# Performance work log

Measured on AMD Instinct MI355X. Metric: run time of the kernel, lower is better.

The kernel has to match this reference:

```python
import jax, jax.numpy as jnp
import numpy as np

D_MODEL = 256; N_HEADS = 8; N_LEVELS = 4; N_POINTS = 4; D_FFN = 1024
SHAPES = [(128, 128), (64, 64), (32, 32), (16, 16)]  # (H, W) per level, strides 8/16/32/64 of 1024x1024 input
B = 8; LQ = 1024
S_TOT = sum(h * w for h, w in SHAPES)


def setup_inputs() -> dict:
    key = jax.random.key(0)
    ks = iter(jax.random.split(key, 48))
    d = D_MODEL

    def f(shape, s=0.02):
        return jax.random.normal(next(ks), shape, dtype=jnp.float32) * s

    return {
        'tgt': f((B, LQ, d), 1.0),
        'query_pos': f((B, LQ, d), 1.0),
        'reference_points': jax.random.uniform(next(ks), (B, LQ, N_LEVELS, 2), dtype=jnp.float32),
        'src': f((B, S_TOT, d), 1.0),
        'w_in': f((3 * d, d)), 'b_in': jnp.zeros((3 * d,), jnp.float32),
        'w_out': f((d, d)), 'b_out': jnp.zeros((d,), jnp.float32),
        'ln1_g': jnp.ones((d,), jnp.float32), 'ln1_b': jnp.zeros((d,), jnp.float32),
        'ln2_g': jnp.ones((d,), jnp.float32), 'ln2_b': jnp.zeros((d,), jnp.float32),
        'ln3_g': jnp.ones((d,), jnp.float32), 'ln3_b': jnp.zeros((d,), jnp.float32),
        'w_val': f((d, d)), 'b_val': jnp.zeros((d,), jnp.float32),
        'w_off': f((N_HEADS * N_LEVELS * N_POINTS * 2, d), 0.002),
        'b_off': f((N_HEADS * N_LEVELS * N_POINTS * 2,), 0.5),
        'w_attw': f((N_HEADS * N_LEVELS * N_POINTS, d)),
        'b_attw': jnp.zeros((N_HEADS * N_LEVELS * N_POINTS,), jnp.float32),
        'w_oc': f((d, d)), 'b_oc': jnp.zeros((d,), jnp.float32),
        'w1': f((D_FFN, d)), 'b1': jnp.zeros((D_FFN,), jnp.float32),
        'w2': f((d, D_FFN)), 'b2': jnp.zeros((d,), jnp.float32),
        'spatial_shapes': jnp.array(SHAPES, dtype=jnp.int32),
    }


def layer_norm(x, g, b):
    mu = x.mean(-1, keepdims=True)
    var = ((x - mu) ** 2).mean(-1, keepdims=True)
    return (x - mu) * jax.lax.rsqrt(var + 1e-5) * g + b


def mha(tgt, query_pos, w_in, b_in, w_out, b_out):
    d = D_MODEL; Dh = d // N_HEADS
    Bs, Lq, _ = tgt.shape
    qk = tgt + query_pos
    q = (qk @ w_in[:d].T + b_in[:d]).reshape(Bs, Lq, N_HEADS, Dh)
    k = (qk @ w_in[d:2 * d].T + b_in[d:2 * d]).reshape(Bs, Lq, N_HEADS, Dh)
    v = (tgt @ w_in[2 * d:].T + b_in[2 * d:]).reshape(Bs, Lq, N_HEADS, Dh)
    attn = jax.nn.softmax(jnp.einsum('bqhd,bkhd->bhqk', q, k) / np.sqrt(Dh).astype(np.float32), axis=-1)
    o = jnp.einsum('bhqk,bkhd->bqhd', attn, v).reshape(Bs, Lq, d)
    return o @ w_out.T + b_out


def ms_deform_attn(value, loc, attw):
    # value [B,S,H,Dh]; loc [B,Lq,H,L,P,2] in [0,1]; attw [B,Lq,H,L,P]
    Bs, _, Hh, Dh = value.shape
    Lq = loc.shape[1]

    def to_hfirst(x):  # [B,Lq,Hh,P] -> [B,Hh,Lq*P,1]
        return jnp.transpose(x, (0, 2, 1, 3)).reshape(Bs, Hh, Lq * N_POINTS, 1)

    acc = jnp.zeros((Bs, Hh, Lq * N_POINTS, Dh), value.dtype)
    start = 0
    for l, (H_, W_) in enumerate(SHAPES):
        v = jnp.transpose(value[:, start:start + H_ * W_], (0, 2, 1, 3))  # [B,Hh,HW,Dh]
        start += H_ * W_
        ll = loc[:, :, :, l]  # [B,Lq,Hh,P,2]
        x = ll[..., 0] * W_ - 0.5
        y = ll[..., 1] * H_ - 0.5
        x0 = jnp.floor(x); y0 = jnp.floor(y)
        tx = x - x0; ty = y - y0

        def gather(xi, yi):
            valid = ((xi >= 0) & (xi < W_) & (yi >= 0) & (yi < H_)).astype(value.dtype)
            fi = (jnp.clip(yi, 0, H_ - 1) * W_ + jnp.clip(xi, 0, W_ - 1)).astype(jnp.int32)
            g = jnp.take_along_axis(v, to_hfirst(fi.astype(jnp.float32)).astype(jnp.int32), axis=2)
            return g * to_hfirst(valid)

        samp = (gather(x0, y0) * to_hfirst((1 - tx) * (1 - ty))
                + gather(x0 + 1, y0) * to_hfirst(tx * (1 - ty))
                + gather(x0, y0 + 1) * to_hfirst((1 - tx) * ty)
                + gather(x0 + 1, y0 + 1) * to_hfirst(tx * ty))
        acc = acc + samp * to_hfirst(attw[:, :, :, l])
    out = acc.reshape(Bs, Hh, Lq, N_POINTS, Dh).sum(3)  # [B,Hh,Lq,Dh]
    return jnp.transpose(out, (0, 2, 1, 3)).reshape(Bs, Lq, Hh * Dh)


def reference(tgt, query_pos, reference_points, src, w_in, b_in, w_out, b_out,
              ln1_g, ln1_b, ln2_g, ln2_b, ln3_g, ln3_b,
              w_val, b_val, w_off, b_off, w_attw, b_attw, w_oc, b_oc,
              w1, b1, w2, b2, spatial_shapes):
    Bs, Lq, d = tgt.shape
    Dh = d // N_HEADS
    # --- self attention (q=k=tgt+pos, v=tgt), residual + norm2 ---
    t2 = mha(tgt, query_pos, w_in, b_in, w_out, b_out)
    tgt = layer_norm(tgt + t2, ln2_g, ln2_b)
    # --- MSDeformAttn cross attention, residual + norm1 ---
    query = tgt + query_pos
    value = (src @ w_val.T + b_val).reshape(Bs, -1, N_HEADS, Dh)
    off = (query @ w_off.T + b_off).reshape(Bs, Lq, N_HEADS, N_LEVELS, N_POINTS, 2)
    aw = jax.nn.softmax((query @ w_attw.T + b_attw).reshape(Bs, Lq, N_HEADS, N_LEVELS * N_POINTS), axis=-1)
    aw = aw.reshape(Bs, Lq, N_HEADS, N_LEVELS, N_POINTS)
    normalizer = jnp.array([[w, h] for h, w in SHAPES], dtype=tgt.dtype)  # (W,H) per level
    loc = reference_points[:, :, None, :, None, :] + off / normalizer[None, None, None, :, None, :]
    ca = ms_deform_attn(value, loc, aw) @ w_oc.T + b_oc
    tgt = layer_norm(tgt + ca, ln1_g, ln1_b)
    # --- FFN, residual + norm3 ---
    t2 = jax.nn.relu(tgt @ w1.T + b1) @ w2.T + b2
    tgt = layer_norm(tgt + t2, ln3_g, ln3_b)
    return tgt
```

## Files before the change

### kernel.cpp

```cpp
#include <hip/hip_runtime.h>

typedef unsigned short ushort_t;
typedef unsigned int uint_t;
typedef __attribute__((ext_vector_type(8))) short short8;
typedef __attribute__((ext_vector_type(4))) float floatx4;
typedef __attribute__((ext_vector_type(4))) unsigned short ushortx4;

__device__ __forceinline__ ushort_t f2bf(float f){
  uint_t u = __builtin_bit_cast(uint_t, f);
  u += 0x7FFFu + ((u >> 16) & 1u);
  return (ushort_t)(u >> 16);
}
__device__ __forceinline__ float bf2f(ushort_t u){
  uint_t x = ((uint_t)u) << 16;
  return __builtin_bit_cast(float, x);
}
__device__ __forceinline__ uint_t packbf2(float a, float b){
  return (uint_t)f2bf(a) | ((uint_t)f2bf(b) << 16);
}

__device__ __forceinline__ void gload16(const void* g, void* l){
  __builtin_amdgcn_global_load_lds(
      (const __attribute__((address_space(1))) void*)g,
      (__attribute__((address_space(3))) void*)l, 16, 0, 0);
}

#define FENCED_BARRIER() asm volatile("s_barrier" ::: "memory")

__global__ __launch_bounds__(256) void convert_w_kernel(const float* __restrict__ w_in_v,
    const float* __restrict__ w_val, const float* __restrict__ w_out,
    const float* __restrict__ w_oc, const float* __restrict__ w1,
    const float* __restrict__ w2, ushort_t* __restrict__ dst){
  int j = (blockIdx.x*256 + threadIdx.x) * 4;
  if (j >= 786432) return;
  const float* src; int off;
  if      (j <  65536){ src = w_in_v; off = 0;      }
  else if (j < 131072){ src = w_val;  off = 65536;  }
  else if (j < 196608){ src = w_out;  off = 131072; }
  else if (j < 262144){ src = w_oc;   off = 196608; }
  else if (j < 524288){ src = w1;     off = 262144; }
  else                { src = w2;     off = 524288; }
  float4 v = *(const float4*)(src + (j - off));
  uint2 u; u.x = packbf2(v.x, v.y); u.y = packbf2(v.z, v.w);
  *(uint2*)(dst + j) = u;
}

__global__ __launch_bounds__(256) void pack_offattw_kernel(const float* __restrict__ w_off,
    const float* __restrict__ w_attw, const float* __restrict__ b_off,
    const float* __restrict__ b_attw, float* __restrict__ dst){
  int j = (blockIdx.x*256 + threadIdx.x) * 4;
  if (j >= 98688) return;
  const float* src; int off;
  if      (j < 65536){ src = w_off;  off = 0;     }
  else if (j < 98304){ src = w_attw; off = 65536; }
  else if (j < 98560){ src = b_off;  off = 98304; }
  else               { src = b_attw; off = 98560; }
  *(float4*)(dst + j) = *(const float4*)(src + (j - off));
}

__global__ __launch_bounds__(256) void addln_kernel(const float* __restrict__ X,
    const float* __restrict__ Y, const float* __restrict__ gw,
    const float* __restrict__ bw, float* __restrict__ Out){
  int wave = threadIdx.x >> 6, lane = threadIdx.x & 63;
  long row = (long)blockIdx.x * 4 + wave;
  long base = row * 256 + lane * 4;
  float4 x = *(const float4*)(X + base);
  float4 y = *(const float4*)(Y + base);
  float v0=x.x+y.x, v1=x.y+y.y, v2=x.z+y.z, v3=x.w+y.w;
  float s  = v0+v1+v2+v3;
  float sq = v0*v0+v1*v1+v2*v2+v3*v3;
  #pragma unroll
  for (int off=32; off>0; off>>=1){
    s  += __shfl_xor(s, off);
    sq += __shfl_xor(sq, off);
  }
  float mu  = s * (1.f/256.f);
  float var = sq * (1.f/256.f) - mu*mu;
  float rs  = rsqrtf(var + 1e-5f);
  float4 g4 = *(const float4*)(gw + lane*4);
  float4 b4 = *(const float4*)(bw + lane*4);
  float4 o;
  o.x = (v0-mu)*rs*g4.x + b4.x;
  o.y = (v1-mu)*rs*g4.y + b4.y;
  o.z = (v2-mu)*rs*g4.z + b4.z;
  o.w = (v3-mu)*rs*g4.w + b4.w;
  *(float4*)(Out + base) = o;
}

__device__ __forceinline__ void stage_store(ushort_t* ls, int r, int c4, float4 v){
  int byte = r*64 + ((((c4>>1) ^ ((r>>1)&3)) << 4) | ((c4&1) << 3));
  uint2 u; u.x = packbf2(v.x, v.y); u.y = packbf2(v.z, v.w);
  *(uint2*)((char*)ls + byte) = u;
}
__device__ __forceinline__ void stage_copy16(ushort_t* ls, int r, int s, short8 v){
  int byte = r*64 + ((s ^ ((r>>1)&3)) << 4);
  *(short8*)((char*)ls + byte) = v;
}
__device__ __forceinline__ short8 frag_load(const ushort_t* ls, int r, int g){
  int byte = r*64 + ((g ^ ((r>>1)&3)) << 4);
  return *(const short8*)((const char*)ls + byte);
}

__device__ __forceinline__ short8 frag_load_f32(const float* ls, int r, int g){
  const char* base = (const char*)ls + r*128;
  int x = r & 7;
  float4 f0 = *(const float4*)(base + ((((2*g)  ^ x)) << 4));
  float4 f1 = *(const float4*)(base + ((((2*g+1)^ x)) << 4));
  uint4 u;
  u.x = packbf2(f0.x, f0.y); u.y = packbf2(f0.z, f0.w);
  u.z = packbf2(f1.x, f1.y); u.w = packbf2(f1.z, f1.w);
  return __builtin_bit_cast(short8, u);
}

template<bool RELU, bool OUT_BF16>
__global__ __launch_bounds__(256) void gemm_dma3_kernel(const float* __restrict__ A,
    const ushort_t* __restrict__ Wbf, const float* __restrict__ bias,
    void* __restrict__ Cout, int M, int N, int K){
  __shared__ float    ldsA[2][2048];
  __shared__ ushort_t ldsB[2][4096];
  const int t = threadIdx.x;
  const int lane = t & 63, wave = t >> 6;
  const int wm = wave >> 1, wn = wave & 1;
  const long rowA0 = (long)blockIdx.x * 64;
  const long rowB0 = (long)blockIdx.y * 128;
  const int rr = lane & 15, g = lane >> 4;
  const int arow_in = lane >> 3;
  const int aslot   = (lane & 7) ^ (arow_in & 7);
  const int brow_in = lane >> 2;
  const int bslot   = lane & 3;
  floatx4 acc[2][4] = {};
  const int nsteps = K >> 5;

  #define ISSUE3(kk, buf) do { \
    _Pragma("unroll") \
    for (int c=0;c<2;++c){ \
      int ar_ = wave*16 + c*8 + arow_in; \
      gload16(A + (rowA0 + ar_)*(long)K + (kk) + aslot*4, \
              &ldsA[buf][(wave*16 + c*8)*32]); \
    } \
    _Pragma("unroll") \
    for (int c=0;c<2;++c){ \
      int br_ = wave*32 + c*16 + brow_in; \
      const ushort_t* bs_ = Wbf + (rowB0 + br_)*(long)K + (kk) + (bslot ^ ((br_>>1)&3))*8; \
      gload16(bs_, (char*)ldsB[buf] + (wave*32 + c*16)*64); \
    } \
  } while(0)

  ISSUE3(0, 0);
  if (nsteps > 1) ISSUE3(32, 1);

  for (int k = 0; k < nsteps; ++k){
    if (k < nsteps-1) asm volatile("s_waitcnt vmcnt(4)" ::: "memory");
    else              asm volatile("s_waitcnt vmcnt(0)" ::: "memory");
    FENCED_BARRIER();
    const float*    lA = ldsA[k & 1];
    const ushort_t* lB = ldsB[k & 1];
    short8 af[2], bfr[4];
    #pragma unroll
    for (int mi=0;mi<2;++mi) af[mi]  = frag_load_f32(lA, wm*32 + mi*16 + rr, g);
    #pragma unroll
    for (int ni=0;ni<4;++ni) bfr[ni] = frag_load(lB, wn*64 + ni*16 + rr, g);
    #pragma unroll
    for (int mi=0;mi<2;++mi)
      #pragma unroll
      for (int ni=0;ni<4;++ni)
        acc[mi][ni] = __builtin_amdgcn_mfma_f32_16x16x32_bf16(af[mi], bfr[ni], acc[mi][ni], 0, 0, 0);
    FENCED_BARRIER();
    if (k + 2 < nsteps) ISSUE3((k+2)*32, k & 1);
  }
  #undef ISSUE3

  const int cg = lane >> 4;
  #pragma unroll
  for (int ni=0;ni<4;++ni){
    long n = rowB0 + wn*64 + ni*16 + (lane & 15);
    float bv = bias[n];
    #pragma unroll
    for (int mi=0;mi<2;++mi){
      long m = rowA0 + wm*32 + mi*16 + cg*4;
      #pragma unroll
      for (int r2=0;r2<4;++r2){
        float v = acc[mi][ni][r2] + bv;
        if (RELU) v = fmaxf(v, 0.f);
        if (OUT_BF16) ((ushort_t*)Cout)[(m+r2)*N + n] = f2bf(v);
        else          ((float*)Cout)[(m+r2)*N + n] = v;
      }
    }
  }
}

template<bool RELU, bool OUT_BF16>
__global__ __launch_bounds__(512, 4) void gemm_dma2_kernel(const float* __restrict__ A,
    const ushort_t* __restrict__ Wbf, const float* __restrict__ bias,
    void* __restrict__ Cout, int M, int N, int K){
  __shared__ float    ldsA[2][4096];
  __shared__ ushort_t ldsB[2][8192];
  const int t = threadIdx.x;
  const int lane = t & 63, wave = t >> 6;
  const int wm = wave >> 2, wn = wave & 3;
  const long rowA0 = (long)blockIdx.x * 128;
  const long n0 = (long)blockIdx.y * 256;
  const int rr = lane & 15, g = lane >> 4;
  const int arow_in = lane >> 3;
  const int aslot   = (lane & 7) ^ (arow_in & 7);
  const int brow_in = lane >> 2;
  const int bslot   = lane & 3;
  floatx4 acc[4][4] = {};
  const int nsteps = K >> 5;

  #define ISSUE2(kk, buf) do { \
    _Pragma("unroll") \
    for (int c=0;c<2;++c){ \
      int ar_ = (wave*2 + c)*8 + arow_in; \
      gload16(A + (rowA0 + ar_)*(long)K + (kk) + aslot*4, \
              &ldsA[buf][(wave*2 + c)*8*32]); \
    } \
    _Pragma("unroll") \
    for (int c=0;c<2;++c){ \
      int br_ = (wave*2 + c)*16 + brow_in; \
      const ushort_t* bs_ = Wbf + (n0 + br_)*(long)K + (kk) + (bslot ^ ((br_>>1)&3))*8; \
      gload16(bs_, (char*)ldsB[buf] + (wave*2 + c)*16*64); \
    } \
  } while(0)

  ISSUE2(0, 0);
  if (nsteps > 1) ISSUE2(32, 1);

  for (int k = 0; k < nsteps; ++k){
    if (k < nsteps-1) asm volatile("s_waitcnt vmcnt(4)" ::: "memory");
    else              asm volatile("s_waitcnt vmcnt(0)" ::: "memory");
    FENCED_BARRIER();
    const float*    lA = ldsA[k & 1];
    const ushort_t* lB = ldsB[k & 1];
    short8 af[4], bfr[4];
    #pragma unroll
    for (int mi=0;mi<4;++mi) af[mi]  = frag_load_f32(lA, wm*64 + mi*16 + rr, g);
    #pragma unroll
    for (int ni=0;ni<4;++ni) bfr[ni] = frag_load(lB, wn*64 + ni*16 + rr, g);
    #pragma unroll
    for (int mi=0;mi<4;++mi)
      #pragma unroll
      for (int ni=0;ni<4;++ni)
        acc[mi][ni] = __builtin_amdgcn_mfma_f32_16x16x32_bf16(af[mi], bfr[ni], acc[mi][ni], 0, 0, 0);
    FENCED_BARRIER();
    if (k + 2 < nsteps) ISSUE2((k+2)*32, k & 1);
  }
  #undef ISSUE2

  const int cg = lane >> 4;
  #pragma unroll
  for (int ni=0;ni<4;++ni){
    long n = n0 + wn*64 + ni*16 + (lane & 15);
    float bv = bias[n];
    #pragma unroll
    for (int mi=0;mi<4;++mi){
      long m = rowA0 + wm*64 + mi*16 + cg*4;
      #pragma unroll
      for (int r2=0;r2<4;++r2){
        float v = acc[mi][ni][r2] + bv;
        if (RELU) v = fmaxf(v, 0.f);
        if (OUT_BF16) ((ushort_t*)Cout)[(m+r2)*N + n] = f2bf(v);
        else          ((float*)Cout)[(m+r2)*N + n] = v;
      }
    }
  }
}

template<bool RELU, bool OUT_BF16>
__global__ __launch_bounds__(256) void gemm_add2_kernel(const float* __restrict__ A,
    const float* __restrict__ A2, const float* __restrict__ W,
    const float* __restrict__ bias, void* __restrict__ Cout,
    int M, int N, int K){
  __shared__ ushort_t lsA[4096], lsB[4096];
  const int t = threadIdx.x;
  const int lane = t & 63, wave = t >> 6;
  const int wm = wave >> 1, wn = wave & 1;
  const long rowA0 = (long)blockIdx.x * 128;
  const long rowB0 = (long)blockIdx.y * 128;
  floatx4 acc[4][4] = {};
  const int rr = lane & 15, g = lane >> 4;
  const int rA = t >> 3, c4 = t & 7;
  const float* Ap = A + (rowA0 + rA)*(long)K + c4*4;
  const float* A2p = A2 + (rowA0 + rA)*(long)K + c4*4;
  const float* Wp = W + (rowB0 + rA)*(long)K + c4*4;

  for (int k0 = 0; k0 < K; k0 += 32){
    __syncthreads();
    #pragma unroll
    for (int j=0;j<4;++j){
      float4 v = *(const float4*)(Ap + k0 + (long)(32*j)*K);
      float4 y = *(const float4*)(A2p + k0 + (long)(32*j)*K);
      v.x+=y.x; v.y+=y.y; v.z+=y.z; v.w+=y.w;
      stage_store(lsA, rA + 32*j, c4, v);
      stage_store(lsB, rA + 32*j, c4, *(const float4*)(Wp + k0 + (long)(32*j)*K));
    }
    __syncthreads();
    short8 af[4], bfr[4];
    #pragma unroll
    for (int mi=0;mi<4;++mi) af[mi]  = frag_load(lsA, wm*64 + mi*16 + rr, g);
    #pragma unroll
    for (int ni=0;ni<4;++ni) bfr[ni] = frag_load(lsB, wn*64 + ni*16 + rr, g);
    #pragma unroll
    for (int mi=0;mi<4;++mi)
      #pragma unroll
      for (int ni=0;ni<4;++ni)
        acc[mi][ni] = __builtin_amdgcn_mfma_f32_16x16x32_bf16(af[mi], bfr[ni], acc[mi][ni], 0, 0, 0);
  }
  const int cg = lane >> 4;
  #pragma unroll
  for (int ni=0;ni<4;++ni){
    long n = rowB0 + wn*64 + ni*16 + (lane & 15);
    float bv = bias[n];
    #pragma unroll
    for (int mi=0;mi<4;++mi){
      long m = rowA0 + wm*64 + mi*16 + cg*4;
      #pragma unroll
      for (int r2=0;r2<4;++r2){
        float v = acc[mi][ni][r2] + bv;
        if (RELU) v = fmaxf(v, 0.f);
        if (OUT_BF16) ((ushort_t*)Cout)[(m+r2)*N + n] = f2bf(v);
        else          ((float*)Cout)[(m+r2)*N + n] = v;
      }
    }
  }
}

__global__ __launch_bounds__(256) void attn_mfma_kernel(const ushort_t* __restrict__ QK,
    const ushort_t* __restrict__ V, float* __restrict__ O){
  __shared__ ushort_t lsQ[4096];
  __shared__ ushort_t lsK[1024];
  __shared__ ushort_t lsVT[1024];
  __shared__ ushort_t lsP[4096];
  const int bh = blockIdx.y, b = bh >> 3, h = bh & 7;
  const int qt0 = blockIdx.x * 128;
  const int t = threadIdx.x, lane = t & 63, w = t >> 6;
  const int rr = lane & 15, g = lane >> 4;
  const float csc = 0.25506332f;

  const ushort_t* qbase = QK + ((long)b*1024 + qt0)*512 + h*32;
  #pragma unroll
  for (int j=0;j<2;++j){
    int i = t + j*256; int r = i>>2, s = i&3;
    short8 v = *(const short8*)(qbase + (long)r*512 + s*8);
    stage_copy16(lsQ, r, s, v);
  }
  __syncthreads();
  short8 bq[2];
  bq[0] = frag_load(lsQ, w*32 + rr, g);
  bq[1] = frag_load(lsQ, w*32 + 16 + rr, g);

  floatx4 accO[2][2] = {};
  float rsum[2] = {0.f, 0.f};
  const ushort_t* kbase = QK + (long)b*1024*512 + 256 + h*32;
  const ushort_t* vbase = V  + (long)b*1024*256 + h*32;

  for (int kt = 0; kt < 1024; kt += 32){
    __syncthreads();
    if (t < 128){
      int r = t >> 2, s = t & 3;
      short8 v = *(const short8*)(kbase + (long)(kt + r)*512 + s*8);
      stage_copy16(lsK, r, s, v);
    }
    {
      int kk = t >> 3, d4 = t & 7;
      ushortx4 vv = *(const ushortx4*)(vbase + (long)(kt + kk)*256 + d4*4);
      #pragma unroll
      for (int j=0;j<4;++j){
        int d = d4*4 + j;
        int cb = kk*2;
        int byte = d*64 + ((((cb>>4) ^ ((d>>1)&3)) << 4) | (cb & 15));
        *(ushort_t*)((char*)lsVT + byte) = vv[j];
      }
    }
    __syncthreads();
    floatx4 accS[2][2] = {};
    short8 ak0 = frag_load(lsK, rr, g);
    short8 ak1 = frag_load(lsK, 16 + rr, g);
    accS[0][0] = __builtin_amdgcn_mfma_f32_16x16x32_bf16(ak0, bq[0], accS[0][0], 0,0,0);
    accS[0][1] = __builtin_amdgcn_mfma_f32_16x16x32_bf16(ak0, bq[1], accS[0][1], 0,0,0);
    accS[1][0] = __builtin_amdgcn_mfma_f32_16x16x32_bf16(ak1, bq[0], accS[1][0], 0,0,0);
    accS[1][1] = __builtin_amdgcn_mfma_f32_16x16x32_bf16(ak1, bq[1], accS[1][1], 0,0,0);
    #pragma unroll
    for (int mi=0;mi<2;++mi){
      #pragma unroll
      for (int ni=0;ni<2;++ni){
        float p0 = exp2f(accS[mi][ni][0]*csc);
        float p1 = exp2f(accS[mi][ni][1]*csc);
        float p2 = exp2f(accS[mi][ni][2]*csc);
        float p3 = exp2f(accS[mi][ni][3]*csc);
        rsum[ni] += (p0+p1)+(p2+p3);
        int q   = w*32 + ni*16 + rr;
        int k0b = (mi*16 + g*4)*2;
        int byte = q*64 + ((((k0b>>4) ^ ((q>>1)&3)) << 4) | (k0b & 15));
        uint2 u; u.x = packbf2(p0,p1); u.y = packbf2(p2,p3);
        *(uint2*)((char*)lsP + byte) = u;
      }
    }
    short8 av0 = frag_load(lsVT, rr, g);
    short8 av1 = frag_load(lsVT, 16 + rr, g);
    short8 bp0 = frag_load(lsP, w*32 + rr, g);
    short8 bp1 = frag_load(lsP, w*32 + 16 + rr, g);
    accO[0][0] = __builtin_amdgcn_mfma_f32_16x16x32_bf16(av0, bp0, accO[0][0], 0,0,0);
    accO[0][1] = __builtin_amdgcn_mfma_f32_16x16x32_bf16(av0, bp1, accO[0][1], 0,0,0);
    accO[1][0] = __builtin_amdgcn_mfma_f32_16x16x32_bf16(av1, bp0, accO[1][0], 0,0,0);
    accO[1][1] = __builtin_amdgcn_mfma_f32_16x16x32_bf16(av1, bp1, accO[1][1], 0,0,0);
  }
  #pragma unroll
  for (int ni=0;ni<2;++ni){
    rsum[ni] += __shfl_xor(rsum[ni], 16);
    rsum[ni] += __shfl_xor(rsum[ni], 32);
    float inv = 1.f / rsum[ni];
    int q = qt0 + w*32 + ni*16 + rr;
    float* op = O + ((long)b*1024 + q)*256 + h*32;
    #pragma unroll
    for (int mi=0;mi<2;++mi){
      #pragma unroll
      for (int r2=0;r2<4;++r2){
        int d = mi*16 + g*4 + r2;
        op[d] = accO[mi][ni][r2] * inv;
      }
    }
  }
}

__global__ __launch_bounds__(256) void deform_kernel(const ushort_t* __restrict__ val,
    const float* __restrict__ offaw, const float* __restrict__ refp,
    float* __restrict__ Out){
  __shared__ float s_cat[1536], s_ref[32];
  const int t = threadIdx.x;
  const long q0 = (long)blockIdx.x * 4;
  const float* srcOA = offaw + q0*384;
  *(float4*)(s_cat + t*4) = *(const float4*)(srcOA + t*4);
  if (t < 128) *(float4*)(s_cat + 1024 + t*4) = *(const float4*)(srcOA + 1024 + t*4);
  if (t < 32)  s_ref[t] = refp[q0*8 + t];
  __syncthreads();
  const int qi = t >> 6, tl = t & 63;
  const int h = tl >> 3, dq = (tl & 7) << 2;
  const int bq = (int)q0 + qi;
  const int b = bq >> 10;
  const float* offp = s_cat + qi*384 + h*32;
  const float* awp  = s_cat + qi*384 + 256 + h*16;
  const float* refq = s_ref + qi*8;
  float mx = -1e30f;
  #pragma unroll
  for (int i=0;i<16;++i) mx = fmaxf(mx, awp[i]);
  float p[16], sum = 0.f;
  #pragma unroll
  for (int i=0;i<16;++i){ p[i] = expf(awp[i]-mx); sum += p[i]; }
  float inv = 1.f/sum;
  const long vb = (long)b*21760*256 + h*32 + dq;
  const int Dim[4] = {128,64,32,16};
  const int St[4]  = {0,16384,20480,21504};
  float a0=0.f, a1=0.f, a2=0.f, a3=0.f;
  #pragma unroll
  for (int l=0;l<4;++l){
    const int Wl = Dim[l], Hl = Dim[l], st = St[l];
    float rx = refq[2*l], ry = refq[2*l+1];
    #pragma unroll
    for (int pp=0;pp<4;++pp){
      float x = rx*(float)Wl + offp[l*8+pp*2]   - 0.5f;
      float y = ry*(float)Hl + offp[l*8+pp*2+1] - 0.5f;
      float xf = floorf(x), yf = floorf(y);
      int x0 = (int)xf, y0 = (int)yf;
      float tx = x - xf, ty = y - yf;
      float s0=0.f,s1=0.f,s2=0.f,s3=0.f;
      #define CORNER(XI, YI, WGT) { \
        int xi_ = (XI), yi_ = (YI); \
        bool valid_ = (xi_ >= 0) & (xi_ < Wl) & (yi_ >= 0) & (yi_ < Hl); \
        int xc_ = min(max(xi_, 0), Wl-1), yc_ = min(max(yi_, 0), Hl-1); \
        ushortx4 u = *(const ushortx4*)(val + vb + (long)(st + yc_*Wl + xc_)*256); \
        float wq = valid_ ? (WGT) : 0.f; \
        s0 += wq*bf2f(u[0]); s1 += wq*bf2f(u[1]); \
        s2 += wq*bf2f(u[2]); s3 += wq*bf2f(u[3]); \
      }
      CORNER(x0,   y0,   (1.f-tx)*(1.f-ty));
      CORNER(x0+1, y0,   tx*(1.f-ty));
      CORNER(x0,   y0+1, (1.f-tx)*ty);
      CORNER(x0+1, y0+1, tx*ty);
      #undef CORNER
      float pw = p[l*4+pp];
      a0 += pw*s0; a1 += pw*s1; a2 += pw*s2; a3 += pw*s3;
    }
  }
  float4 o; o.x=a0*inv; o.y=a1*inv; o.z=a2*inv; o.w=a3*inv;
  *(float4*)(Out + (long)bq*256 + h*32 + dq) = o;
}

extern "C" void kernel_launch(void* const* d_in, const int* in_sizes, int n_in,
                              void* d_out, int out_size, void* d_ws, size_t ws_size,
                              hipStream_t stream){
  (void)in_sizes; (void)n_in; (void)out_size; (void)ws_size;
  const float* tgt   = (const float*)d_in[0];
  const float* qpos  = (const float*)d_in[1];
  const float* refp  = (const float*)d_in[2];
  const float* src   = (const float*)d_in[3];
  const float* w_in  = (const float*)d_in[4];
  const float* b_in  = (const float*)d_in[5];
  const float* w_out = (const float*)d_in[6];
  const float* b_out = (const float*)d_in[7];
  const float* ln1g  = (const float*)d_in[8];
  const float* ln1b  = (const float*)d_in[9];
  const float* ln2g  = (const float*)d_in[10];
  const float* ln2b  = (const float*)d_in[11];
  const float* ln3g  = (const float*)d_in[12];
  const float* ln3b  = (const float*)d_in[13];
  const float* w_val = (const float*)d_in[14];
  const float* b_val = (const float*)d_in[15];
  const float* w_off = (const float*)d_in[16];
  const float* b_off = (const float*)d_in[17];
  const float* w_attw= (const float*)d_in[18];
  const float* b_attw= (const float*)d_in[19];
  const float* w_oc  = (const float*)d_in[20];
  const float* b_oc  = (const float*)d_in[21];
  const float* w1    = (const float*)d_in[22];
  const float* b1    = (const float*)d_in[23];
  const float* w2    = (const float*)d_in[24];
  const float* b2    = (const float*)d_in[25];

  float* ws = (float*)d_ws;
  ushort_t* bufQK = (ushort_t*)(ws + 2097152);
  float* bufOA  = ws + 2097152;
  ushort_t* bufV = (ushort_t*)(ws + 6291456);
  float* bufO   = ws + 8388608;
  float* bufT2  = ws + 10485760;
  float* bufTg1 = ws + 12582912;
  float* bufTg2 = ws + 14680064;
  ushort_t* bufVal = (ushort_t*)(ws + 16777216);
  float* bufH   = ws + 16777216;
  ushort_t* bufWbf = (ushort_t*)(ws + 39059456);
  float* bufWOA = ws + 39452672;
  float* outF   = (float*)d_out;

  const ushort_t* winvbf = bufWbf;
  const ushort_t* wvalbf = bufWbf + 65536;
  const ushort_t* woutbf = bufWbf + 131072;
  const ushort_t* wocbf  = bufWbf + 196608;
  const ushort_t* w1bf   = bufWbf + 262144;
  const ushort_t* w2bf   = bufWbf + 524288;

  dim3 B256(256), B512(512);
  convert_w_kernel<<<dim3(768), B256, 0, stream>>>(w_in + 512*256, w_val, w_out, w_oc, w1, w2, bufWbf);
  pack_offattw_kernel<<<dim3(97), B256, 0, stream>>>(w_off, w_attw, b_off, b_attw, bufWOA);
  gemm_add2_kernel<false,true><<<dim3(64,4), B256, 0, stream>>>(tgt, qpos, w_in, b_in, bufQK, 8192, 512, 256);
  gemm_dma3_kernel<false,true><<<dim3(128,2), B256, 0, stream>>>(tgt, winvbf, b_in + 512, bufV, 8192, 256, 256);
  attn_mfma_kernel<<<dim3(8,64), B256, 0, stream>>>(bufQK, bufV, bufO);
  gemm_dma3_kernel<false,false><<<dim3(128,2), B256, 0, stream>>>(bufO, woutbf, b_out, bufT2, 8192, 256, 256);
  addln_kernel<<<dim3(2048), B256, 0, stream>>>(tgt, bufT2, ln2g, ln2b, bufTg1);
  gemm_dma2_kernel<false,true><<<dim3(1360,1), B512, 0, stream>>>(src, wvalbf, b_val, bufVal, 174080, 256, 256);
  gemm_add2_kernel<false,false><<<dim3(64,3), B256, 0, stream>>>(bufTg1, qpos, bufWOA, bufWOA + 98304, bufOA, 8192, 384, 256);
  deform_kernel<<<dim3(2048), B256, 0, stream>>>(bufVal, bufOA, refp, bufO);
  gemm_dma3_kernel<false,false><<<dim3(128,2), B256, 0, stream>>>(bufO, wocbf, b_oc, bufT2, 8192, 256, 256);
  addln_kernel<<<dim3(2048), B256, 0, stream>>>(bufTg1, bufT2, ln1g, ln1b, bufTg2);
  gemm_dma2_kernel<true,false><<<dim3(64,4), B512, 0, stream>>>(bufTg2, w1bf, b1, bufH, 8192, 1024, 256);
  gemm_dma3_kernel<false,false><<<dim3(128,2), B256, 0, stream>>>(bufH, w2bf, b2, bufT2, 8192, 256, 1024);
  addln_kernel<<<dim3(2048), B256, 0, stream>>>(bufTg2, bufT2, ln3g, ln3b, outF);
}
```

Baseline: 290.9 us.

## Replace GEMM kernels with triple-buffered 64-row DMA GEMM and bf16 pre-converted weights

Replaces the 512-thread double-buffered GEMM with a 256-thread, 64-row-tile, triple-buffered variant for the value projection and FFN1. It also drops the register-staged gemm_add2 path: tgt+pos sums now go through a separate elementwise add kernel, and all weights (including in-proj and offset/attention-weight projections) are pre-converted to bf16 so the DMA GEMM can be used everywhere. The goal is deeper load pipelining and more blocks for latency hiding. The cost is extra add-kernel launches and extra global traffic for the materialised sums.

```diff
diff --git a/kernel.cpp b/kernel.cpp
--- a/kernel.cpp
+++ b/kernel.cpp
@@ -27,35 +27,43 @@
 
 #define FENCED_BARRIER() asm volatile("s_barrier" ::: "memory")
 
-__global__ __launch_bounds__(256) void convert_w_kernel(const float* __restrict__ w_in_v,
+__global__ __launch_bounds__(256) void convert_w_kernel(const float* __restrict__ w_in,
     const float* __restrict__ w_val, const float* __restrict__ w_out,
     const float* __restrict__ w_oc, const float* __restrict__ w1,
-    const float* __restrict__ w2, ushort_t* __restrict__ dst){
+    const float* __restrict__ w2, const float* __restrict__ w_off,
+    const float* __restrict__ w_attw, ushort_t* __restrict__ dst){
   int j = (blockIdx.x*256 + threadIdx.x) * 4;
-  if (j >= 786432) return;
+  if (j >= 1015808) return;
   const float* src; int off;
-  if      (j <  65536){ src = w_in_v; off = 0;      }
-  else if (j < 131072){ src = w_val;  off = 65536;  }
-  else if (j < 196608){ src = w_out;  off = 131072; }
-  else if (j < 262144){ src = w_oc;   off = 196608; }
-  else if (j < 524288){ src = w1;     off = 262144; }
-  else                { src = w2;     off = 524288; }
+  if      (j < 196608){ src = w_in;   off = 0;      }
+  else if (j < 262144){ src = w_val;  off = 196608; }
+  else if (j < 327680){ src = w_out;  off = 262144; }
+  else if (j < 393216){ src = w_oc;   off = 327680; }
+  else if (j < 655360){ src = w1;     off = 393216; }
+  else if (j < 917504){ src = w2;     off = 655360; }
+  else if (j < 983040){ src = w_off;  off = 917504; }
+  else                { src = w_attw; off = 983040; }
   float4 v = *(const float4*)(src + (j - off));
   uint2 u; u.x = packbf2(v.x, v.y); u.y = packbf2(v.z, v.w);
   *(uint2*)(dst + j) = u;
 }
 
-__global__ __launch_bounds__(256) void pack_offattw_kernel(const float* __restrict__ w_off,
-    const float* __restrict__ w_attw, const float* __restrict__ b_off,
+__global__ __launch_bounds__(256) void pack_bias_kernel(const float* __restrict__ b_off,
     const float* __restrict__ b_attw, float* __restrict__ dst){
-  int j = (blockIdx.x*256 + threadIdx.x) * 4;
-  if (j >= 98688) return;
-  const float* src; int off;
-  if      (j < 65536){ src = w_off;  off = 0;     }
-  else if (j < 98304){ src = w_attw; off = 65536; }
-  else if (j < 98560){ src = b_off;  off = 98304; }
-  else               { src = b_attw; off = 98560; }
-  *(float4*)(dst + j) = *(const float4*)(src + (j - off));
+  int t = threadIdx.x;
+  dst[t] = b_off[t];
+  if (t < 128) dst[256 + t] = b_attw[t];
+}
+
+__global__ __launch_bounds__(256) void add_kernel(const float* __restrict__ a,
+    const float* __restrict__ b, float* __restrict__ c, int n4){
+  int i = blockIdx.x * 256 + threadIdx.x;
+  if (i < n4){
+    float4 x = ((const float4*)a)[i];
+    float4 y = ((const float4*)b)[i];
+    float4 z; z.x=x.x+y.x; z.y=x.y+y.y; z.z=x.z+y.z; z.w=x.w+y.w;
+    ((float4*)c)[i] = z;
+  }
 }
 
 __global__ __launch_bounds__(256) void addln_kernel(const float* __restrict__ X,
@@ -87,11 +95,6 @@
   *(float4*)(Out + base) = o;
 }
 
-__device__ __forceinline__ void stage_store(ushort_t* ls, int r, int c4, float4 v){
-  int byte = r*64 + ((((c4>>1) ^ ((r>>1)&3)) << 4) | ((c4&1) << 3));
-  uint2 u; u.x = packbf2(v.x, v.y); u.y = packbf2(v.z, v.w);
-  *(uint2*)((char*)ls + byte) = u;
-}
 __device__ __forceinline__ void stage_copy16(ushort_t* ls, int r, int s, short8 v){
   int byte = r*64 + ((s ^ ((r>>1)&3)) << 4);
   *(short8*)((char*)ls + byte) = v;
@@ -190,16 +193,15 @@
 }
 
 template<bool RELU, bool OUT_BF16>
-__global__ __launch_bounds__(512, 4) void gemm_dma2_kernel(const float* __restrict__ A,
+__global__ __launch_bounds__(256) void gemm_dma4_kernel(const float* __restrict__ A,
     const ushort_t* __restrict__ Wbf, const float* __restrict__ bias,
     void* __restrict__ Cout, int M, int N, int K){
-  __shared__ float    ldsA[2][4096];
-  __shared__ ushort_t ldsB[2][8192];
+  __shared__ float    ldsA[3][2048];
+  __shared__ ushort_t ldsB[3][8192];
   const int t = threadIdx.x;
   const int lane = t & 63, wave = t >> 6;
-  const int wm = wave >> 2, wn = wave & 3;
-  const long rowA0 = (long)blockIdx.x * 128;
-  const long n0 = (long)blockIdx.y * 256;
+  const long rowA0 = (long)blockIdx.x * 64;
+  const long rowB0 = (long)blockIdx.y * 256;
   const int rr = lane & 15, g = lane >> 4;
   const int arow_in = lane >> 3;
   const int aslot   = (lane & 7) ^ (arow_in & 7);
@@ -208,112 +210,57 @@
   floatx4 acc[4][4] = {};
   const int nsteps = K >> 5;
 
-  #define ISSUE2(kk, buf) do { \
+  #define ISSUE4(kk, buf) do { \
     _Pragma("unroll") \
     for (int c=0;c<2;++c){ \
-      int ar_ = (wave*2 + c)*8 + arow_in; \
+      int ar_ = wave*16 + c*8 + arow_in; \
       gload16(A + (rowA0 + ar_)*(long)K + (kk) + aslot*4, \
-              &ldsA[buf][(wave*2 + c)*8*32]); \
+              &ldsA[buf][(wave*16 + c*8)*32]); \
     } \
     _Pragma("unroll") \
-    for (int c=0;c<2;++c){ \
-      int br_ = (wave*2 + c)*16 + brow_in; \
-      const ushort_t* bs_ = Wbf + (n0 + br_)*(long)K + (kk) + (bslot ^ ((br_>>1)&3))*8; \
-      gload16(bs_, (char*)ldsB[buf] + (wave*2 + c)*16*64); \
+    for (int c=0;c<4;++c){ \
+      int br_ = wave*64 + c*16 + brow_in; \
+      const ushort_t* bs_ = Wbf + (rowB0 + br_)*(long)K + (kk) + (bslot ^ ((br_>>1)&3))*8; \
+      gload16(bs_, (char*)ldsB[buf] + (wave*64 + c*16)*64); \
     } \
   } while(0)
 
-  ISSUE2(0, 0);
-  if (nsteps > 1) ISSUE2(32, 1);
+  ISSUE4(0, 0);
+  if (nsteps > 1) ISSUE4(32, 1);
+  if (nsteps > 2) ISSUE4(64, 2);
 
   for (int k = 0; k < nsteps; ++k){
-    if (k < nsteps-1) asm volatile("s_waitcnt vmcnt(4)" ::: "memory");
-    else              asm volatile("s_waitcnt vmcnt(0)" ::: "memory");
+    int ahead = nsteps - 1 - k; if (ahead > 2) ahead = 2;
+    if (ahead == 2)      asm volatile("s_waitcnt vmcnt(12)" ::: "memory");
+    else if (ahead == 1) asm volatile("s_waitcnt vmcnt(6)"  ::: "memory");
+    else                 asm volatile("s_waitcnt vmcnt(0)"  ::: "memory");
     FENCED_BARRIER();
-    const float*    lA = ldsA[k & 1];
-    const ushort_t* lB = ldsB[k & 1];
+    int bsel = k % 3;
+    const float*    lA = ldsA[bsel];
+    const ushort_t* lB = ldsB[bsel];
     short8 af[4], bfr[4];
     #pragma unroll
-    for (int mi=0;mi<4;++mi) af[mi]  = frag_load_f32(lA, wm*64 + mi*16 + rr, g);
-    #pragma unroll
-    for (int ni=0;ni<4;++ni) bfr[ni] = frag_load(lB, wn*64 + ni*16 + rr, g);
+    for (int mi=0;mi<4;++mi) af[mi]  = frag_load_f32(lA, mi*16 + rr, g);
+    #pragma unroll
+    for (int ni=0;ni<4;++ni) bfr[ni] = frag_load(lB, wave*64 + ni*16 + rr, g);
     #pragma unroll
     for (int mi=0;mi<4;++mi)
       #pragma unroll
       for (int ni=0;ni<4;++ni)
         acc[mi][ni] = __builtin_amdgcn_mfma_f32_16x16x32_bf16(af[mi], bfr[ni], acc[mi][ni], 0, 0, 0);
     FENCED_BARRIER();
-    if (k + 2 < nsteps) ISSUE2((k+2)*32, k & 1);
-  }
-  #undef ISSUE2
+    if (k + 3 < nsteps) ISSUE4((k+3)*32, bsel);
+  }
+  #undef ISSUE4
 
   const int cg = lane >> 4;
   #pragma unroll
   for (int ni=0;ni<4;++ni){
-    long n = n0 + wn*64 + ni*16 + (lane & 15);
+    long n = rowB0 + wave*64 + ni*16 + (lane & 15);
     float bv = bias[n];
     #pragma unroll
     for (int mi=0;mi<4;++mi){
-      long m = rowA0 + wm*64 + mi*16 + cg*4;
-      #pragma unroll
-      for (int r2=0;r2<4;++r2){
-        float v = acc[mi][ni][r2] + bv;
-        if (RELU) v = fmaxf(v, 0.f);
-        if (OUT_BF16) ((ushort_t*)Cout)[(m+r2)*N + n] = f2bf(v);
-        else          ((float*)Cout)[(m+r2)*N + n] = v;
-      }
-    }
-  }
-}
-
-template<bool RELU, bool OUT_BF16>
-__global__ __launch_bounds__(256) void gemm_add2_kernel(const float* __restrict__ A,
-    const float* __restrict__ A2, const float* __restrict__ W,
-    const float* __restrict__ bias, void* __restrict__ Cout,
-    int M, int N, int K){
-  __shared__ ushort_t lsA[4096], lsB[4096];
-  const int t = threadIdx.x;
-  const int lane = t & 63, wave = t >> 6;
-  const int wm = wave >> 1, wn = wave & 1;
-  const long rowA0 = (long)blockIdx.x * 128;
-  const long rowB0 = (long)blockIdx.y * 128;
-  floatx4 acc[4][4] = {};
-  const int rr = lane & 15, g = lane >> 4;
-  const int rA = t >> 3, c4 = t & 7;
-  const float* Ap = A + (rowA0 + rA)*(long)K + c4*4;
-  const float* A2p = A2 + (rowA0 + rA)*(long)K + c4*4;
-  const float* Wp = W + (rowB0 + rA)*(long)K + c4*4;
-
-  for (int k0 = 0; k0 < K; k0 += 32){
-    __syncthreads();
-    #pragma unroll
-    for (int j=0;j<4;++j){
-      float4 v = *(const float4*)(Ap + k0 + (long)(32*j)*K);
-      float4 y = *(const float4*)(A2p + k0 + (long)(32*j)*K);
-      v.x+=y.x; v.y+=y.y; v.z+=y.z; v.w+=y.w;
-      stage_store(lsA, rA + 32*j, c4, v);
-      stage_store(lsB, rA + 32*j, c4, *(const float4*)(Wp + k0 + (long)(32*j)*K));
-    }
-    __syncthreads();
-    short8 af[4], bfr[4];
-    #pragma unroll
-    for (int mi=0;mi<4;++mi) af[mi]  = frag_load(lsA, wm*64 + mi*16 + rr, g);
-    #pragma unroll
-    for (int ni=0;ni<4;++ni) bfr[ni] = frag_load(lsB, wn*64 + ni*16 + rr, g);
-    #pragma unroll
-    for (int mi=0;mi<4;++mi)
-      #pragma unroll
-      for (int ni=0;ni<4;++ni)
-        acc[mi][ni] = __builtin_amdgcn_mfma_f32_16x16x32_bf16(af[mi], bfr[ni], acc[mi][ni], 0, 0, 0);
-  }
-  const int cg = lane >> 4;
-  #pragma unroll
-  for (int ni=0;ni<4;++ni){
-    long n = rowB0 + wn*64 + ni*16 + (lane & 15);
-    float bv = bias[n];
-    #pragma unroll
-    for (int mi=0;mi<4;++mi){
-      long m = rowA0 + wm*64 + mi*16 + cg*4;
+      long m = rowA0 + mi*16 + cg*4;
       #pragma unroll
       for (int r2=0;r2<4;++r2){
         float v = acc[mi][ni][r2] + bv;
@@ -518,40 +465,45 @@
   const float* b2    = (const float*)d_in[25];
 
   float* ws = (float*)d_ws;
-  ushort_t* bufQK = (ushort_t*)(ws + 2097152);
-  float* bufOA  = ws + 2097152;
-  ushort_t* bufV = (ushort_t*)(ws + 6291456);
-  float* bufO   = ws + 8388608;
-  float* bufT2  = ws + 10485760;
-  float* bufTg1 = ws + 12582912;
-  float* bufTg2 = ws + 14680064;
+  ushort_t* bufWbf = (ushort_t*)ws;
+  float* bufBOA = ws + 507904;
+  float* bufQ   = ws + 524288;
+  float* bufOA  = ws + 524288;
+  ushort_t* bufQK = (ushort_t*)(ws + 2621440);
+  ushort_t* bufV  = (ushort_t*)(ws + 4718592);
+  float* bufO   = ws + 5767168;
+  float* bufT2  = ws + 7864320;
+  float* bufTg1 = ws + 9961472;
+  float* bufTg2 = ws + 12058624;
   ushort_t* bufVal = (ushort_t*)(ws + 16777216);
   float* bufH   = ws + 16777216;
-  ushort_t* bufWbf = (ushort_t*)(ws + 39059456);
-  float* bufWOA = ws + 39452672;
   float* outF   = (float*)d_out;
 
-  const ushort_t* winvbf = bufWbf;
-  const ushort_t* wvalbf = bufWbf + 65536;
-  const ushort_t* woutbf = bufWbf + 131072;
-  const ushort_t* wocbf  = bufWbf + 196608;
-  const ushort_t* w1bf   = bufWbf + 262144;
-  const ushort_t* w2bf   = bufWbf + 524288;
-
-  dim3 B256(256), B512(512);
-  convert_w_kernel<<<dim3(768), B256, 0, stream>>>(w_in + 512*256, w_val, w_out, w_oc, w1, w2, bufWbf);
-  pack_offattw_kernel<<<dim3(97), B256, 0, stream>>>(w_off, w_attw, b_off, b_attw, bufWOA);
-  gemm_add2_kernel<false,true><<<dim3(64,4), B256, 0, stream>>>(tgt, qpos, w_in, b_in, bufQK, 8192, 512, 256);
+  const ushort_t* winbf    = bufWbf;
+  const ushort_t* winvbf   = bufWbf + 131072;
+  const ushort_t* wvalbf   = bufWbf + 196608;
+  const ushort_t* woutbf   = bufWbf + 262144;
+  const ushort_t* wocbf    = bufWbf + 327680;
+  const ushort_t* w1bf     = bufWbf + 393216;
+  const ushort_t* w2bf     = bufWbf + 655360;
+  const ushort_t* woffawbf = bufWbf + 917504;
+
+  dim3 B256(256);
+  convert_w_kernel<<<dim3(992), B256, 0, stream>>>(w_in, w_val, w_out, w_oc, w1, w2, w_off, w_attw, bufWbf);
+  pack_bias_kernel<<<dim3(1), B256, 0, stream>>>(b_off, b_attw, bufBOA);
+  add_kernel<<<dim3(2048), B256, 0, stream>>>(tgt, qpos, bufQ, 524288);
+  gemm_dma3_kernel<false,true><<<dim3(128,4), B256, 0, stream>>>(bufQ, winbf, b_in, bufQK, 8192, 512, 256);
   gemm_dma3_kernel<false,true><<<dim3(128,2), B256, 0, stream>>>(tgt, winvbf, b_in + 512, bufV, 8192, 256, 256);
   attn_mfma_kernel<<<dim3(8,64), B256, 0, stream>>>(bufQK, bufV, bufO);
   gemm_dma3_kernel<false,false><<<dim3(128,2), B256, 0, stream>>>(bufO, woutbf, b_out, bufT2, 8192, 256, 256);
   addln_kernel<<<dim3(2048), B256, 0, stream>>>(tgt, bufT2, ln2g, ln2b, bufTg1);
-  gemm_dma2_kernel<false,true><<<dim3(1360,1), B512, 0, stream>>>(src, wvalbf, b_val, bufVal, 174080, 256, 256);
-  gemm_add2_kernel<false,false><<<dim3(64,3), B256, 0, stream>>>(bufTg1, qpos, bufWOA, bufWOA + 98304, bufOA, 8192, 384, 256);
+  gemm_dma4_kernel<false,true><<<dim3(2720,1), B256, 0, stream>>>(src, wvalbf, b_val, bufVal, 174080, 256, 256);
+  add_kernel<<<dim3(2048), B256, 0, stream>>>(bufTg1, qpos, bufT2, 524288);
+  gemm_dma3_kernel<false,false><<<dim3(128,3), B256, 0, stream>>>(bufT2, woffawbf, bufBOA, bufOA, 8192, 384, 256);
   deform_kernel<<<dim3(2048), B256, 0, stream>>>(bufVal, bufOA, refp, bufO);
   gemm_dma3_kernel<false,false><<<dim3(128,2), B256, 0, stream>>>(bufO, wocbf, b_oc, bufT2, 8192, 256, 256);
   addln_kernel<<<dim3(2048), B256, 0, stream>>>(bufTg1, bufT2, ln1g, ln1b, bufTg2);
-  gemm_dma2_kernel<true,false><<<dim3(64,4), B512, 0, stream>>>(bufTg2, w1bf, b1, bufH, 8192, 1024, 256);
+  gemm_dma4_kernel<true,false><<<dim3(128,4), B256, 0, stream>>>(bufTg2, w1bf, b1, bufH, 8192, 1024, 256);
   gemm_dma3_kernel<false,false><<<dim3(128,2), B256, 0, stream>>>(bufH, w2bf, b2, bufT2, 8192, 256, 1024);
   addln_kernel<<<dim3(2048), B256, 0, stream>>>(bufTg2, bufT2, ln3g, ln3b, outF);
 }
```

Result: slower. 298.2 us (+2.5%).
